# Kernel optimization log

Measured on AMD Instinct MI355X. Metric: run time of the kernel, lower is better.

## Reference

```python
import jax, jax.numpy as jnp
import numpy as np

N, E = 100000, 250000
SD, CD = 128, 768


def setup_inputs() -> dict:
    key = jax.random.key(0)
    ks = jax.random.split(key, 12)
    z = jax.random.normal(ks[0], (N, SD), dtype=jnp.float32)
    chemistry = jax.random.normal(ks[1], (N, CD), dtype=jnp.float32)
    edge = jax.random.randint(ks[2], (E, 2), 0, N, dtype=jnp.int64)
    smiles_mask = (jax.random.uniform(ks[3], (N,)) < 0.8).astype(jnp.float32)
    s = 1.0 / np.sqrt(SD)
    W1s = jax.random.uniform(ks[4], (SD, SD // 2), jnp.float32, -s, s)
    b1s = jax.random.uniform(ks[5], (SD // 2,), jnp.float32, -s, s)
    s2 = 1.0 / np.sqrt(SD // 2)
    W2s = jax.random.uniform(ks[6], (SD // 2, 1), jnp.float32, -s2, s2)
    b2s = jax.random.uniform(ks[7], (1,), jnp.float32, -s2, s2)
    c = 1.0 / np.sqrt(CD)
    W1c = jax.random.uniform(ks[8], (CD, CD // 4), jnp.float32, -c, c)
    b1c = jax.random.uniform(ks[9], (CD // 4,), jnp.float32, -c, c)
    c2 = 1.0 / np.sqrt(CD // 4)
    W2c = jax.random.uniform(ks[10], (CD // 4, 1), jnp.float32, -c2, c2)
    b2c = jax.random.uniform(ks[11], (1,), jnp.float32, -c2, c2)
    alpha = jnp.float32(0.1)
    return {"z": z, "chemistry": chemistry, "edge": edge, "smiles_mask": smiles_mask,
            "W1s": W1s, "b1s": b1s, "W2s": W2s, "b2s": b2s,
            "W1c": W1c, "b1c": b1c, "W2c": W2c, "b2c": b2c, "alpha": alpha}


def reference(z, chemistry, edge, smiles_mask, W1s, b1s, W2s, b2s,
              W1c, b1c, W2c, b2c, alpha):
    src, dst = edge[:, 0], edge[:, 1]
    # structural branch: gather, product, 2-layer MLP (dropout = eval identity)
    structural_prod = z[src] * z[dst]                      # [E, SD]
    h_s = jax.nn.relu(structural_prod @ W1s + b1s)         # [E, SD//2]
    score_structural = (h_s @ W2s + b2s)[:, 0]             # [E]
    # chemical branch
    chemical_prod = chemistry[src] * chemistry[dst]        # [E, CD]
    h_c = jax.nn.relu(chemical_prod @ W1c + b1c)           # [E, CD//4]
    score_chemical = (h_c @ W2c + b2c)[:, 0]               # [E]
    both_valid = smiles_mask[src] * smiles_mask[dst]       # [E]
    score_chemical = both_valid * score_chemical
    return score_structural + alpha * score_chemical
```

## Files before the change

### kernel.cpp

```cpp
#include <hip/hip_runtime.h>
#include <hip/hip_bf16.h>
#include <stdint.h>

#define N_NODES 100000
#define NE      250000
#define SDIM    128
#define CDIM    768
#define HS      64
#define HC      192
#define TILE_E  32
#define NBLK    ((NE + TILE_E - 1) / TILE_E)

#define CT2     32
#define NT2     ((NE + CT2 - 1) / CT2)
#define CBLK2   256

typedef __attribute__((ext_vector_type(8))) short bf16x8;
typedef __attribute__((ext_vector_type(4))) float f32x4;

static __device__ __forceinline__ uint16_t f2bf(float f) {
    union { __hip_bfloat16 h; uint16_t u; } cv;
    cv.h = __float2bfloat16(f);
    return cv.u;
}
static __device__ __forceinline__ float bf2f(uint16_t u) {
    union { float f; uint32_t i; } cv; cv.i = ((uint32_t)u) << 16; return cv.f;
}

__global__ void k_convert_w(const float* __restrict__ W1c, uint16_t* __restrict__ W1cT) {
    const int tid = blockIdx.x * 256 + threadIdx.x;
    const int stride = gridDim.x * 256;
    for (int i = tid; i < HC * CDIM; i += stride) {
        const int n = i / CDIM, k = i - n * CDIM;
        W1cT[i] = f2bf(W1c[k * HC + n]);
    }
}

__global__ __launch_bounds__(256, 3) void k_structural(
    const float* __restrict__ z, const int* __restrict__ edge,
    const float* __restrict__ W1s, const float* __restrict__ b1s,
    const float* __restrict__ W2s, const float* __restrict__ b2s,
    const float* __restrict__ smask, const float* __restrict__ alphap,
    float* __restrict__ out, float* __restrict__ valid,
    const float* __restrict__ chem, uint16_t* __restrict__ chem_bf, long conv_n)
{
    __shared__ float Wl[SDIM * HS];
    __shared__ float Pl[TILE_E * 132];

    const int t = threadIdx.x;
    const int e0 = blockIdx.x * TILE_E;

    {
        const float4* src = (const float4*)W1s;
        float4* dst = (float4*)Wl;
        for (int m = t; m < SDIM * HS / 4; m += 256) dst[m] = src[m];
    }
    {
        const int el = t >> 3, p = t & 7;
        const int e = e0 + el;
        if (e < NE) {
            const int s = edge[2 * e], d = edge[2 * e + 1];
            const float* rs = z + (long)s * SDIM;
            const float* rd = z + (long)d * SDIM;
            #pragma unroll
            for (int cc = 0; cc < 2; ++cc) {
                const int c = p + cc * 8;
                float4 s0 = *(const float4*)(rs + c * 8);
                float4 s1 = *(const float4*)(rs + c * 8 + 4);
                float4 d0 = *(const float4*)(rd + c * 8);
                float4 d1 = *(const float4*)(rd + c * 8 + 4);
                float4 r0 = {s0.x * d0.x, s0.y * d0.y, s0.z * d0.z, s0.w * d0.w};
                float4 r1 = {s1.x * d1.x, s1.y * d1.y, s1.z * d1.z, s1.w * d1.w};
                *(float4*)(&Pl[el * 132 + c * 8]) = r0;
                *(float4*)(&Pl[el * 132 + c * 8 + 4]) = r1;
            }
        }
    }
    __syncthreads();

    const int el = t >> 3, p = t & 7;
    float h[8] = {0, 0, 0, 0, 0, 0, 0, 0};
    const float4* Wl4 = (const float4*)Wl;
    #pragma unroll 4
    for (int k = 0; k < SDIM; ++k) {
        const float pv = Pl[el * 132 + k];
        float4 w0 = Wl4[k * 16 + p * 2];
        float4 w1 = Wl4[k * 16 + p * 2 + 1];
        h[0] += pv * w0.x; h[1] += pv * w0.y; h[2] += pv * w0.z; h[3] += pv * w0.w;
        h[4] += pv * w1.x; h[5] += pv * w1.y; h[6] += pv * w1.z; h[7] += pv * w1.w;
    }
    float partial = 0.f;
    #pragma unroll
    for (int j = 0; j < 8; ++j) {
        const int c = p * 8 + j;
        partial += fmaxf(h[j] + b1s[c], 0.f) * W2s[c];
    }
    partial += __shfl_xor(partial, 1);
    partial += __shfl_xor(partial, 2);
    partial += __shfl_xor(partial, 4);
    const int e = e0 + el;
    if (p == 0 && e < NE) {
        out[e] = partial + b2s[0];
        const int s = edge[2 * e], d = edge[2 * e + 1];
        valid[e] = alphap[0] * smask[s] * smask[d];
    }

    {
        const long base = ((long)blockIdx.x * 256 + t) * 8;
        const long stride = (long)gridDim.x * 256 * 8;
        for (long i = base; i < conv_n; i += stride) {
            float4 a = *(const float4*)(chem + i);
            float4 b = *(const float4*)(chem + i + 4);
            union { uint16_t u[8]; int4 v; } pk;
            pk.u[0] = f2bf(a.x); pk.u[1] = f2bf(a.y);
            pk.u[2] = f2bf(a.z); pk.u[3] = f2bf(a.w);
            pk.u[4] = f2bf(b.x); pk.u[5] = f2bf(b.y);
            pk.u[6] = f2bf(b.z); pk.u[7] = f2bf(b.w);
            *(int4*)(chem_bf + i) = pk.v;
        }
    }
}

static __device__ __forceinline__ void cvt_store_bf(uint16_t* Abuf, int el, int ch,
                                                    int4 vs, int4 vd) {
    union { int4 v; uint16_t u[8]; } a, b, r;
    a.v = vs; b.v = vd;
    #pragma unroll
    for (int q = 0; q < 8; ++q) r.u[q] = f2bf(bf2f(a.u[q]) * bf2f(b.u[q]));
    const int byte = el * 1536 + ((ch * 16) ^ ((el & 7) << 4));
    *(int4*)((char*)Abuf + byte) = r.v;
}
static __device__ __forceinline__ void zero_store(uint16_t* Abuf, int el, int ch) {
    const int byte = el * 1536 + ((ch * 16) ^ ((el & 7) << 4));
    int4 z = {0, 0, 0, 0};
    *(int4*)((char*)Abuf + byte) = z;
}
static __device__ __forceinline__ void stage_f32(uint16_t* Abuf, int el, int ch,
                                                 const float* rs, const float* rd) {
    float4 a0 = *(const float4*)(rs + ch * 8);
    float4 a1 = *(const float4*)(rs + ch * 8 + 4);
    float4 b0 = *(const float4*)(rd + ch * 8);
    float4 b1 = *(const float4*)(rd + ch * 8 + 4);
    union { int4 v; uint16_t u[8]; } r;
    r.u[0] = f2bf(a0.x * b0.x); r.u[1] = f2bf(a0.y * b0.y);
    r.u[2] = f2bf(a0.z * b0.z); r.u[3] = f2bf(a0.w * b0.w);
    r.u[4] = f2bf(a1.x * b1.x); r.u[5] = f2bf(a1.y * b1.y);
    r.u[6] = f2bf(a1.z * b1.z); r.u[7] = f2bf(a1.w * b1.w);
    const int byte = el * 1536 + ((ch * 16) ^ ((el & 7) << 4));
    *(int4*)((char*)Abuf + byte) = r.v;
}

template<bool BF16TAB>
__global__ __launch_bounds__(768, 3) void k_chem_v4(
    const void* __restrict__ chemv, const int* __restrict__ edge,
    const uint16_t* __restrict__ W1cT, const float* __restrict__ b1c,
    const float* __restrict__ W2c, const float* __restrict__ b2c,
    const float* __restrict__ valid, float* __restrict__ out)
{
    __shared__ uint16_t A[2][CT2 * CDIM];
    __shared__ float xchg[6][64][20];
    __shared__ float part[2][CT2][8];

    const int t = threadIdx.x;
    const int w = t >> 6, lane = t & 63, lr = lane & 15, lg = lane >> 4;
    const int cg = w >> 1, kh = w & 1;
    const int b = blockIdx.x;

    const int t0 = b * 30 + (b < 133 ? b : 133);
    const int t1 = t0 + 30 + (b < 133 ? 1 : 0);

    const uint16_t* chemB = (const uint16_t*)chemv;
    const float*    chemF = (const float*)chemv;

    bf16x8 Breg[24];
    #pragma unroll
    for (int ct = 0; ct < 2; ++ct) {
        const uint16_t* Bp = W1cT + (long)(cg * 32 + ct * 16 + lr) * CDIM + kh * 384 + lg * 8;
        #pragma unroll
        for (int kc = 0; kc < 12; ++kc)
            Breg[ct * 12 + kc] = *(const bf16x8*)(Bp + kc * 32);
    }
    float b1v[2], w2v[2];
    #pragma unroll
    for (int ct = 0; ct < 2; ++ct) {
        b1v[ct] = b1c[cg * 32 + ct * 16 + lr];
        w2v[ct] = W2c[cg * 32 + ct * 16 + lr];
    }
    const float b2 = b2c[0];

    const int elb = t / 96;
    const int ch  = t % 96;

    #pragma unroll
    for (int q = 0; q < 4; ++q) {
        const int el = elb + 8 * q;
        const int e  = t0 * CT2 + el;
        const bool ok = (e < NE);
        const int ee = ok ? e : 0;
        const int si = edge[2 * ee], di = edge[2 * ee + 1];
        if constexpr (BF16TAB) {
            int4 vs = *(const int4*)(chemB + (long)si * CDIM + ch * 8);
            int4 vd = *(const int4*)(chemB + (long)di * CDIM + ch * 8);
            if (ok) cvt_store_bf(A[0], el, ch, vs, vd);
            else    zero_store(A[0], el, ch);
        } else {
            if (ok) stage_f32(A[0], el, ch, chemF + (long)si * CDIM, chemF + (long)di * CDIM);
            else    zero_store(A[0], el, ch);
        }
    }

    int2 eid[4];
    #pragma unroll
    for (int q = 0; q < 4; ++q) {
        const int e = (t0 + 1) * CT2 + elb + 8 * q;
        const int ee = (e < NE) ? e : 0;
        eid[q] = *(const int2*)(edge + 2 * ee);
    }

    float vld_cur = 0.f, vld_next = 0.f;
    if (t < CT2) {
        const int e = t0 * CT2 + t;
        vld_next = (e < NE) ? valid[e] : 0.f;
    }
    __syncthreads();

    const int swz = (lr & 7) << 4;
    const int rb0 = lr * 1536;
    const int rb1 = rb0 + 16 * 1536;

    for (int ti = t0; ti < t1; ++ti) {
        const int it = ti - t0, cur = it & 1;
        const bool pf  = (ti + 1 < t1);
        const bool pf2 = (ti + 2 < t1);

        if (pf) {
            uint16_t* dst = A[cur ^ 1];
            const int ebase = (ti + 1) * CT2;
            if constexpr (BF16TAB) {
                {
                    int4 vs0 = *(const int4*)(chemB + (long)eid[0].x * CDIM + ch * 8);
                    int4 vd0 = *(const int4*)(chemB + (long)eid[0].y * CDIM + ch * 8);
                    int4 vs1 = *(const int4*)(chemB + (long)eid[1].x * CDIM + ch * 8);
                    int4 vd1 = *(const int4*)(chemB + (long)eid[1].y * CDIM + ch * 8);
                    if (ebase + elb < NE)     cvt_store_bf(dst, elb,     ch, vs0, vd0);
                    else                      zero_store(dst, elb, ch);
                    if (ebase + elb + 8 < NE) cvt_store_bf(dst, elb + 8, ch, vs1, vd1);
                    else                      zero_store(dst, elb + 8, ch);
                }
                {
                    int4 vs2 = *(const int4*)(chemB + (long)eid[2].x * CDIM + ch * 8);
                    int4 vd2 = *(const int4*)(chemB + (long)eid[2].y * CDIM + ch * 8);
                    int4 vs3 = *(const int4*)(chemB + (long)eid[3].x * CDIM + ch * 8);
                    int4 vd3 = *(const int4*)(chemB + (long)eid[3].y * CDIM + ch * 8);
                    if (ebase + elb + 16 < NE) cvt_store_bf(dst, elb + 16, ch, vs2, vd2);
                    else                       zero_store(dst, elb + 16, ch);
                    if (ebase + elb + 24 < NE) cvt_store_bf(dst, elb + 24, ch, vs3, vd3);
                    else                       zero_store(dst, elb + 24, ch);
                }
            } else {
                #pragma unroll
                for (int q = 0; q < 4; ++q) {
                    const int el = elb + 8 * q;
                    if (ebase + el < NE)
                        stage_f32(dst, el, ch, chemF + (long)eid[q].x * CDIM,
                                  chemF + (long)eid[q].y * CDIM);
                    else zero_store(dst, el, ch);
                }
            }
        }
        int2 eidn[4];
        if (pf2) {
            #pragma unroll
            for (int q = 0; q < 4; ++q) {
                const int e = (ti + 2) * CT2 + elb + 8 * q;
                const int ee = (e < NE) ? e : 0;
                eidn[q] = *(const int2*)(edge + 2 * ee);
            }
        }

        if (ti > t0 && t < CT2) {
            const int e = (ti - 1) * CT2 + t;
            if (e < NE) {
                float s_ = 0.f;
                #pragma unroll
                for (int c6 = 0; c6 < 6; ++c6) s_ += part[cur ^ 1][t][c6];
                atomicAdd(&out[e], vld_cur * (s_ + b2));
            }
        }
        if (t < CT2) {
            vld_cur = vld_next;
            if (pf) {
                const int e = (ti + 1) * CT2 + t;
                vld_next = (e < NE) ? valid[e] : 0.f;
            }
        }

        f32x4 acc00 = {0,0,0,0}, acc01 = {0,0,0,0}, acc10 = {0,0,0,0}, acc11 = {0,0,0,0};
        {
            const char* Ab = (const char*)A[cur];
            #pragma unroll
            for (int kc = 0; kc < 12; ++kc) {
                const int off = ((kh * 12 + kc) * 64 + lg * 16) ^ swz;
                bf16x8 a0 = *(const bf16x8*)(Ab + rb0 + off);
                bf16x8 a1 = *(const bf16x8*)(Ab + rb1 + off);
                acc00 = __builtin_amdgcn_mfma_f32_16x16x32_bf16(a0, Breg[kc],      acc00, 0, 0, 0);
                acc10 = __builtin_amdgcn_mfma_f32_16x16x32_bf16(a1, Breg[kc],      acc10, 0, 0, 0);
                acc01 = __builtin_amdgcn_mfma_f32_16x16x32_bf16(a0, Breg[12 + kc], acc01, 0, 0, 0);
                acc11 = __builtin_amdgcn_mfma_f32_16x16x32_bf16(a1, Breg[12 + kc], acc11, 0, 0, 0);
            }
        }

        if (kh == 1) {
            float* xp = xchg[cg][lane];
            *(float4*)(xp +  0) = (float4){acc00[0], acc00[1], acc00[2], acc00[3]};
            *(float4*)(xp +  4) = (float4){acc01[0], acc01[1], acc01[2], acc01[3]};
            *(float4*)(xp +  8) = (float4){acc10[0], acc10[1], acc10[2], acc10[3]};
            *(float4*)(xp + 12) = (float4){acc11[0], acc11[1], acc11[2], acc11[3]};
        }
        __syncthreads();
        if (kh == 0) {
            const float* xp = xchg[cg][lane];
            float4 x0 = *(const float4*)(xp + 0);
            float4 x1 = *(const float4*)(xp + 4);
            float4 x2 = *(const float4*)(xp + 8);
            float4 x3 = *(const float4*)(xp + 12);
            acc00[0] += x0.x; acc00[1] += x0.y; acc00[2] += x0.z; acc00[3] += x0.w;
            acc01[0] += x1.x; acc01[1] += x1.y; acc01[2] += x1.z; acc01[3] += x1.w;
            acc10[0] += x2.x; acc10[1] += x2.y; acc10[2] += x2.z; acc10[3] += x2.w;
            acc11[0] += x3.x; acc11[1] += x3.y; acc11[2] += x3.z; acc11[3] += x3.w;
            #pragma unroll
            for (int r = 0; r < 4; ++r) {
                float p0 = fmaxf(acc00[r] + b1v[0], 0.f) * w2v[0]
                         + fmaxf(acc01[r] + b1v[1], 0.f) * w2v[1];
                float p1 = fmaxf(acc10[r] + b1v[0], 0.f) * w2v[0]
                         + fmaxf(acc11[r] + b1v[1], 0.f) * w2v[1];
                #pragma unroll
                for (int m = 1; m <= 8; m <<= 1) {
                    p0 += __shfl_xor(p0, m);
                    p1 += __shfl_xor(p1, m);
                }
                if (lr == 0) {
                    part[cur][lg * 4 + r][cg]      = p0;
                    part[cur][16 + lg * 4 + r][cg] = p1;
                }
            }
        }
        __syncthreads();
        if (pf2) { eid[0] = eidn[0]; eid[1] = eidn[1]; eid[2] = eidn[2]; eid[3] = eidn[3]; }
    }

    if (t < CT2) {
        const int e = (t1 - 1) * CT2 + t;
        if (e < NE) {
            const int cur = (t1 - 1 - t0) & 1;
            float s_ = 0.f;
            #pragma unroll
            for (int c6 = 0; c6 < 6; ++c6) s_ += part[cur][t][c6];
            atomicAdd(&out[e], vld_cur * (s_ + b2));
        }
    }
}

extern "C" void kernel_launch(void* const* d_in, const int* in_sizes, int n_in,
                              void* d_out, int out_size, void* d_ws, size_t ws_size,
                              hipStream_t stream)
{
    const float* z     = (const float*)d_in[0];
    const float* chem  = (const float*)d_in[1];
    const int*   edge  = (const int*)d_in[2];
    const float* smask = (const float*)d_in[3];
    const float* W1s   = (const float*)d_in[4];
    const float* b1s   = (const float*)d_in[5];
    const float* W2s   = (const float*)d_in[6];
    const float* b2s   = (const float*)d_in[7];
    const float* W1c   = (const float*)d_in[8];
    const float* b1c   = (const float*)d_in[9];
    const float* W2c   = (const float*)d_in[10];
    const float* b2c   = (const float*)d_in[11];
    const float* alpha = (const float*)d_in[12];
    float* out = (float*)d_out;

    uint16_t* W1cT   = (uint16_t*)d_ws;
    uint16_t* chemBf = (uint16_t*)d_ws + (size_t)HC * CDIM;
    const size_t bfBytes = (size_t)N_NODES * CDIM * 2;
    const size_t needBf  = (size_t)HC * CDIM * 2 + bfBytes + (size_t)NE * 4;
    const bool useBf = ws_size >= needBf;
    float* valid = useBf
        ? (float*)((char*)d_ws + (size_t)HC * CDIM * 2 + bfBytes)
        : (float*)((char*)d_ws + (size_t)HC * CDIM * 2);
    const long conv_n = useBf ? (long)N_NODES * CDIM : 0;

    k_convert_w<<<dim3(64), dim3(256), 0, stream>>>(W1c, W1cT);

    k_structural<<<dim3(NBLK), dim3(256), 0, stream>>>(
        z, edge, W1s, b1s, W2s, b2s, smask, alpha, out, valid, chem, chemBf, conv_n);

    if (useBf)
        k_chem_v4<true><<<dim3(CBLK2), dim3(768), 0, stream>>>(
            (const void*)chemBf, edge, W1cT, b1c, W2c, b2c, valid, out);
    else
        k_chem_v4<false><<<dim3(CBLK2), dim3(768), 0, stream>>>(
            (const void*)chem, edge, W1cT, b1c, W2c, b2c, valid, out);
}
```

Measured before the change: 389.6 us.

## Hoist chemistry gathers above MFMA and stage edge indices through LDS

In the chemical kernel, the global gathers for the next tile are now issued at the top of each iteration into registers. Their conversion and store into the shared-memory A buffer is deferred until after the MFMA/reduction work, so gather latency overlaps compute. Edge index pairs for future tiles are now loaded by 32 threads into a double-buffered LDS array instead of being held in per-thread registers. Occupancy is expressed via amdgpu_waves_per_eu(3,3). The extra 32 live VGPRs across the MFMA section could raise register pressure or cause spills.

```diff
diff --git a/kernel.cpp b/kernel.cpp
--- a/kernel.cpp
+++ b/kernel.cpp
@@ -151,7 +151,8 @@
 }
 
 template<bool BF16TAB>
-__global__ __launch_bounds__(768, 3) void k_chem_v4(
+__global__ __attribute__((amdgpu_waves_per_eu(3, 3))) __launch_bounds__(768)
+void k_chem_v5(
     const void* __restrict__ chemv, const int* __restrict__ edge,
     const uint16_t* __restrict__ W1cT, const float* __restrict__ b1c,
     const float* __restrict__ W2c, const float* __restrict__ b2c,
@@ -160,6 +161,7 @@
     __shared__ uint16_t A[2][CT2 * CDIM];
     __shared__ float xchg[6][64][20];
     __shared__ float part[2][CT2][8];
+    __shared__ int   ebuf[2][2 * CT2];
 
     const int t = threadIdx.x;
     const int w = t >> 6, lane = t & 63, lr = lane & 15, lg = lane >> 4;
@@ -208,15 +210,12 @@
             else    zero_store(A[0], el, ch);
         }
     }
-
-    int2 eid[4];
-    #pragma unroll
-    for (int q = 0; q < 4; ++q) {
-        const int e = (t0 + 1) * CT2 + elb + 8 * q;
+    if (t < CT2) {
+        const int e = (t0 + 1) * CT2 + t;
         const int ee = (e < NE) ? e : 0;
-        eid[q] = *(const int2*)(edge + 2 * ee);
-    }
-
+        int2 p2 = *(const int2*)(edge + 2 * ee);
+        *(int2*)&ebuf[(t0 + 1) & 1][2 * t] = p2;
+    }
     float vld_cur = 0.f, vld_next = 0.f;
     if (t < CT2) {
         const int e = t0 * CT2 + t;
@@ -233,49 +232,27 @@
         const bool pf  = (ti + 1 < t1);
         const bool pf2 = (ti + 2 < t1);
 
-        if (pf) {
-            uint16_t* dst = A[cur ^ 1];
-            const int ebase = (ti + 1) * CT2;
-            if constexpr (BF16TAB) {
-                {
-                    int4 vs0 = *(const int4*)(chemB + (long)eid[0].x * CDIM + ch * 8);
-                    int4 vd0 = *(const int4*)(chemB + (long)eid[0].y * CDIM + ch * 8);
-                    int4 vs1 = *(const int4*)(chemB + (long)eid[1].x * CDIM + ch * 8);
-                    int4 vd1 = *(const int4*)(chemB + (long)eid[1].y * CDIM + ch * 8);
-                    if (ebase + elb < NE)     cvt_store_bf(dst, elb,     ch, vs0, vd0);
-                    else                      zero_store(dst, elb, ch);
-                    if (ebase + elb + 8 < NE) cvt_store_bf(dst, elb + 8, ch, vs1, vd1);
-                    else                      zero_store(dst, elb + 8, ch);
-                }
-                {
-                    int4 vs2 = *(const int4*)(chemB + (long)eid[2].x * CDIM + ch * 8);
-                    int4 vd2 = *(const int4*)(chemB + (long)eid[2].y * CDIM + ch * 8);
-                    int4 vs3 = *(const int4*)(chemB + (long)eid[3].x * CDIM + ch * 8);
-                    int4 vd3 = *(const int4*)(chemB + (long)eid[3].y * CDIM + ch * 8);
-                    if (ebase + elb + 16 < NE) cvt_store_bf(dst, elb + 16, ch, vs2, vd2);
-                    else                       zero_store(dst, elb + 16, ch);
-                    if (ebase + elb + 24 < NE) cvt_store_bf(dst, elb + 24, ch, vs3, vd3);
-                    else                       zero_store(dst, elb + 24, ch);
-                }
-            } else {
-                #pragma unroll
-                for (int q = 0; q < 4; ++q) {
-                    const int el = elb + 8 * q;
-                    if (ebase + el < NE)
-                        stage_f32(dst, el, ch, chemF + (long)eid[q].x * CDIM,
-                                  chemF + (long)eid[q].y * CDIM);
-                    else zero_store(dst, el, ch);
-                }
-            }
-        }
-        int2 eidn[4];
-        if (pf2) {
-            #pragma unroll
-            for (int q = 0; q < 4; ++q) {
-                const int e = (ti + 2) * CT2 + elb + 8 * q;
-                const int ee = (e < NE) ? e : 0;
-                eidn[q] = *(const int2*)(edge + 2 * ee);
-            }
+        int4 vs0, vd0, vs1, vd1, vs2, vd2, vs3, vd3;
+        if (BF16TAB && pf) {
+            const int par = (ti + 1) & 1;
+            int2 e0p = *(const int2*)&ebuf[par][2 * elb];
+            int2 e1p = *(const int2*)&ebuf[par][2 * (elb + 8)];
+            int2 e2p = *(const int2*)&ebuf[par][2 * (elb + 16)];
+            int2 e3p = *(const int2*)&ebuf[par][2 * (elb + 24)];
+            vs0 = *(const int4*)(chemB + (long)e0p.x * CDIM + ch * 8);
+            vd0 = *(const int4*)(chemB + (long)e0p.y * CDIM + ch * 8);
+            vs1 = *(const int4*)(chemB + (long)e1p.x * CDIM + ch * 8);
+            vd1 = *(const int4*)(chemB + (long)e1p.y * CDIM + ch * 8);
+            vs2 = *(const int4*)(chemB + (long)e2p.x * CDIM + ch * 8);
+            vd2 = *(const int4*)(chemB + (long)e2p.y * CDIM + ch * 8);
+            vs3 = *(const int4*)(chemB + (long)e3p.x * CDIM + ch * 8);
+            vd3 = *(const int4*)(chemB + (long)e3p.y * CDIM + ch * 8);
+        }
+        if (pf2 && t < CT2) {
+            const int e = (ti + 2) * CT2 + t;
+            const int ee = (e < NE) ? e : 0;
+            int2 p2 = *(const int2*)(edge + 2 * ee);
+            *(int2*)&ebuf[ti & 1][2 * t] = p2;
         }
 
         if (ti > t0 && t < CT2) {
@@ -345,8 +322,33 @@
                 }
             }
         }
+
+        if (pf) {
+            uint16_t* dst = A[cur ^ 1];
+            const int ebase = (ti + 1) * CT2;
+            if constexpr (BF16TAB) {
+                if (ebase + elb < NE)      cvt_store_bf(dst, elb,      ch, vs0, vd0);
+                else                       zero_store(dst, elb, ch);
+                if (ebase + elb + 8 < NE)  cvt_store_bf(dst, elb + 8,  ch, vs1, vd1);
+                else                       zero_store(dst, elb + 8, ch);
+                if (ebase + elb + 16 < NE) cvt_store_bf(dst, elb + 16, ch, vs2, vd2);
+                else                       zero_store(dst, elb + 16, ch);
+                if (ebase + elb + 24 < NE) cvt_store_bf(dst, elb + 24, ch, vs3, vd3);
+                else                       zero_store(dst, elb + 24, ch);
+            } else {
+                const int par = (ti + 1) & 1;
+                #pragma unroll
+                for (int q = 0; q < 4; ++q) {
+                    const int el = elb + 8 * q;
+                    if (ebase + el < NE) {
+                        int2 p2 = *(const int2*)&ebuf[par][2 * el];
+                        stage_f32(dst, el, ch, chemF + (long)p2.x * CDIM,
+                                  chemF + (long)p2.y * CDIM);
+                    } else zero_store(dst, el, ch);
+                }
+            }
+        }
         __syncthreads();
-        if (pf2) { eid[0] = eidn[0]; eid[1] = eidn[1]; eid[2] = eidn[2]; eid[3] = eidn[3]; }
     }
 
     if (t < CT2) {
@@ -396,9 +398,9 @@
         z, edge, W1s, b1s, W2s, b2s, smask, alpha, out, valid, chem, chemBf, conv_n);
 
     if (useBf)
-        k_chem_v4<true><<<dim3(CBLK2), dim3(768), 0, stream>>>(
+        k_chem_v5<true><<<dim3(CBLK2), dim3(768), 0, stream>>>(
             (const void*)chemBf, edge, W1cT, b1c, W2c, b2c, valid, out);
     else
-        k_chem_v4<false><<<dim3(CBLK2), dim3(768), 0, stream>>>(
+        k_chem_v5<false><<<dim3(CBLK2), dim3(768), 0, stream>>>(
             (const void*)chem, edge, W1cT, b1c, W2c, b2c, valid, out);
 }
```

Measured after the change: 456.3 us. 17.1% more time.
